# Performance work log

Hardware: AMD Instinct MI355X
Metric: run time of the kernel (lower is better)

The kernel has to match this reference:

```python
import jax, jax.numpy as jnp
import numpy as np
import math

DIM, DEPTH, HEADS, VOCAB, DMODEL = 200, 6, 10, 7, 512
DH = DIM // HEADS                      # 20
NBF = int(DH * math.log(DH))           # 59 FAVOR+ random features
FF = 4 * DIM                           # 800


def setup_inputs() -> dict:
    key = jax.random.key(0)
    ks = iter(jax.random.split(key, 32))
    s = 0.02
    inp = {
        'x': jax.random.normal(next(ks), (4, 16, 2048), jnp.float32),
        'token_emb': jax.random.normal(next(ks), (VOCAB, DIM)) * s,
        'ln1_g': jnp.ones((DEPTH, DIM)), 'ln1_b': jnp.zeros((DEPTH, DIM)),
        'wq': jax.random.normal(next(ks), (DEPTH, DIM, DIM)) * s, 'bq': jnp.zeros((DEPTH, DIM)),
        'wk': jax.random.normal(next(ks), (DEPTH, DIM, DIM)) * s, 'bk': jnp.zeros((DEPTH, DIM)),
        'wv': jax.random.normal(next(ks), (DEPTH, DIM, DIM)) * s, 'bv': jnp.zeros((DEPTH, DIM)),
        'proj': jax.random.normal(next(ks), (DEPTH, NBF, DH)),  # FAVOR+ projection (buffer)
        'wo': jax.random.normal(next(ks), (DEPTH, DIM, DIM)) * s, 'bo': jnp.zeros((DEPTH, DIM)),
        'ln2_g': jnp.ones((DEPTH, DIM)), 'ln2_b': jnp.zeros((DEPTH, DIM)),
        'ffw1': jax.random.normal(next(ks), (DEPTH, DIM, FF)) * s, 'ffb1': jnp.zeros((DEPTH, FF)),
        'ffw2': jax.random.normal(next(ks), (DEPTH, FF, DIM)) * s, 'ffb2': jnp.zeros((DEPTH, DIM)),
        'lnf_g': jnp.ones((DIM,)), 'lnf_b': jnp.zeros((DIM,)),
        'proj_w': jax.random.normal(next(ks), (DIM, DMODEL)) * s, 'proj_b': jnp.zeros((DMODEL,)),
    }
    return inp


def layer_norm(x, g, b, eps=1e-5):
    mu = x.mean(-1, keepdims=True)
    var = ((x - mu) ** 2).mean(-1, keepdims=True)
    return (x - mu) / jnp.sqrt(var + eps) * g + b


def softmax_kernel(data, proj, is_query, eps=1e-4):
    # data: (N,H,S,dh); proj: (m,dh)
    dn = data * (data.shape[-1] ** -0.25)
    dash = jnp.einsum('nhsd,md->nhsm', dn, proj)
    diag = 0.5 * jnp.sum(dn * dn, axis=-1, keepdims=True)
    mx = jnp.max(dash, axis=-1, keepdims=True) if is_query else jnp.max(dash)
    return (proj.shape[0] ** -0.5) * (jnp.exp(dash - diag - mx) + eps)


def attention(x, wq, bq, wk, bk, wv, bv, proj, wo, bo):
    N, S, D = x.shape
    split = lambda t: t.reshape(N, S, HEADS, DH).transpose(0, 2, 1, 3)
    q, k, v = split(x @ wq + bq), split(x @ wk + bk), split(x @ wv + bv)
    qp = softmax_kernel(q, proj, True)
    kp = softmax_kernel(k, proj, False)
    d_inv = 1.0 / jnp.einsum('nhsm,nhm->nhs', qp, kp.sum(axis=2))
    ctx = jnp.einsum('nhsm,nhsd->nhmd', kp, v)          # linear attention context
    out = jnp.einsum('nhsm,nhmd->nhsd', qp, ctx) * d_inv[..., None]
    return out.transpose(0, 2, 1, 3).reshape(N, S, D) @ wo + bo


def feedforward(x, w1, b1, w2, b2):
    return jax.nn.gelu(x @ w1 + b1, approximate=False) @ w2 + b2


def performer_forward(tokens, p):
    h = p['token_emb'][tokens]            # pos_emb is zeros (g2v_position_emb=False)
    x1, x2 = h, h                         # reversible net: x duplicated along channels
    for l in range(DEPTH):
        x1 = x1 + attention(layer_norm(x2, p['ln1_g'][l], p['ln1_b'][l]),
                            p['wq'][l], p['bq'][l], p['wk'][l], p['bk'][l],
                            p['wv'][l], p['bv'][l], p['proj'][l], p['wo'][l], p['bo'][l])
        x2 = x2 + feedforward(layer_norm(x1, p['ln2_g'][l], p['ln2_b'][l]),
                              p['ffw1'][l], p['ffb1'][l], p['ffw2'][l], p['ffb2'][l])
    h = 0.5 * (x1 + x2)                   # mean over the two reversible halves
    return layer_norm(h, p['lnf_g'], p['lnf_b'])


def reference(x, token_emb, ln1_g, ln1_b, wq, bq, wk, bk, wv, bv, proj, wo, bo,
              ln2_g, ln2_b, ffw1, ffb1, ffw2, ffb2, lnf_g, lnf_b, proj_w, proj_b):
    p = dict(token_emb=token_emb, ln1_g=ln1_g, ln1_b=ln1_b, wq=wq, bq=bq, wk=wk, bk=bk,
             wv=wv, bv=bv, proj=proj, wo=wo, bo=bo, ln2_g=ln2_g, ln2_b=ln2_b,
             ffw1=ffw1, ffb1=ffb1, ffw2=ffw2, ffb2=ffb2, lnf_g=lnf_g, lnf_b=lnf_b)
    B, Nt, T = x.shape
    xf = x.reshape(B * Nt, T)
    # torch.quantile on 1D positives -> bin_edges shape (1,4) != (T,4), so the
    # original falls back to zero bin edges; edges_plus = [0,0,0,0,inf], hence
    # token = 4 if value > 0 else 0, then + cls_token_id (1).
    tokens = jnp.where(xf > 0, 4, 0).astype(jnp.int32) + 1
    # chunk loop (chunk_size=512 samples) is identity math: run all at once
    enc = performer_forward(tokens, p)    # (B*Nt, T, DIM)
    pooled = enc.mean(axis=1)             # mean-pool over sequence
    out = pooled @ proj_w + proj_b
    return out.reshape(B, Nt, DMODEL)
```

## Files before the change

kernel.cpp:

```cpp
#include <hip/hip_runtime.h>
#include <hip/hip_bf16.h>
#include <math.h>

#define DEPTH   6
#define DIM     200
#define HEADS   10
#define DH      20
#define NBF     59
#define FFD     800
#define DMODEL  512
#define NSEQ    64
#define SEQ     2048
#define NTOK    (NSEQ*SEQ)
#define KPAD    224
#define BUFPAD  64
#define KNROW   40
#define VROW    136
#define KPROW   136
#define QPROW   72
#define CTXR    21
#define HSROW   132
#define PKV_E   (512*KPAD)
#define PQ_E    (256*KPAD)
#define PWO_E   (256*KPAD)
#define PF1_E   (896*KPAD)
#define PF2_E   (256*800)

typedef __hip_bfloat16 bf16;
typedef unsigned short u16;
typedef short s8v __attribute__((ext_vector_type(8)));
typedef short s4v __attribute__((ext_vector_type(4)));
typedef float f4v __attribute__((ext_vector_type(4)));

constexpr float SCALE = 0.4728708045015879f;
constexpr float RATIO = 0.1301889109808239f;
constexpr float KEPS  = 1e-4f;

__device__ __forceinline__ float b2f(bf16 v) { return __bfloat162float(v); }
__device__ __forceinline__ bf16 f2b(float v) { return __float2bfloat16(v); }
__device__ __forceinline__ float bfu(u16 u) {
    return __uint_as_float(((unsigned)u) << 16);
}
__device__ __forceinline__ u16 f2u(float v) {
    bf16 hb = __float2bfloat16(v);
    return *(u16*)&hb;
}
__device__ __forceinline__ float gelu_f(float x) {
    float inner = 0.7978845608028654f * (x + 0.044715f * x * x * x);
    float e = __expf(2.f * inner);
    return x * (1.f - 1.f / (e + 1.f));
}
__device__ __forceinline__ void gld_lds16(const short* g, short* l) {
    __builtin_amdgcn_global_load_lds(
        (const __attribute__((address_space(1))) void*)g,
        (__attribute__((address_space(3))) void*)l, 16, 0, 0);
}
#define MFMA16(a, b, c) __builtin_amdgcn_mfma_f32_16x16x32_bf16(a, b, c, 0, 0, 0)

__global__ void sentinel_kernel(float* out, float wsmb) {
    if (threadIdx.x == 0) out[0] = wsmb;
}

__global__ void zeropad_kernel(bf16* p1, bf16* p2, bf16* p3, bf16* p4) {
    int i = threadIdx.x;
    if (i < BUFPAD) {
        bf16 z = f2b(0.f);
        p1[i] = z; p2[i] = z; p3[i] = z; p4[i] = z;
    }
}

__global__ __launch_bounds__(256) void prep_layer(
        const float* __restrict__ wq, const float* __restrict__ wk,
        const float* __restrict__ wv, const float* __restrict__ wo,
        const float* __restrict__ f1, const float* __restrict__ f2,
        const float* __restrict__ g1, const float* __restrict__ b1,
        const float* __restrict__ g2, const float* __restrict__ b2,
        const float* __restrict__ bq, const float* __restrict__ bk,
        const float* __restrict__ bv, const float* __restrict__ f1b,
        bf16* __restrict__ pKV, bf16* __restrict__ pQ, bf16* __restrict__ pWO,
        bf16* __restrict__ pF1, bf16* __restrict__ pF2,
        float* __restrict__ uw) {
    int b = blockIdx.x, t = threadIdx.x;
    if (b < 448) {
        int idx = b * 256 + t;
        int row = idx / KPAD, k = idx % KPAD;
        float v = 0.f;
        if (k < DIM) {
            if (row < DIM) v = wk[(size_t)k * DIM + row] * g1[k];
            else if (row >= 256 && row < 256 + DIM)
                v = wv[(size_t)k * DIM + (row - 256)] * g1[k];
        }
        pKV[idx] = f2b(v);
    } else if (b < 672) {
        int idx = (b - 448) * 256 + t;
        int row = idx / KPAD, k = idx % KPAD;
        float v = (row < DIM && k < DIM) ? wq[(size_t)k * DIM + row] * g1[k] : 0.f;
        pQ[idx] = f2b(v);
    } else if (b < 896) {
        int idx = (b - 672) * 256 + t;
        int row = idx / KPAD, k = idx % KPAD;
        float v = (row < DIM && k < DIM) ? wo[(size_t)k * DIM + row] : 0.f;
        pWO[idx] = f2b(v);
    } else if (b < 1680) {
        int idx = (b - 896) * 256 + t;
        int row = idx / KPAD, k = idx % KPAD;
        float v = (row < FFD && k < DIM) ? f1[(size_t)k * FFD + row] * g2[k] : 0.f;
        pF1[idx] = f2b(v);
    } else if (b < 2480) {
        int idx = (b - 1680) * 256 + t;
        int row = idx / 800, k = idx % 800;
        float v = (row < DIM) ? f2[(size_t)k * DIM + row] : 0.f;
        pF2[idx] = f2b(v);
    } else if (b < 2482) {
        int j = b - 2480;
        const float* W    = j ? wv : wk;
        const float* bias = j ? bv : bk;
        int n = t;
        float su = 0.f, sw = 0.f;
        if (n < DIM) {
            for (int k = 0; k < DIM; ++k) {
                float wvv = W[(size_t)k * DIM + n];
                su += g1[k] * wvv;
                sw += b1[k] * wvv;
            }
            sw += bias[n];
        }
        uw[j * 256 + n] = su;
        uw[512 + j * 256 + n] = sw;
    } else if (b == 2482) {
        int n = t;
        float su = 0.f, sw = 0.f;
        if (n < DIM) {
            for (int k = 0; k < DIM; ++k) {
                float wvv = wq[(size_t)k * DIM + n];
                su += g1[k] * wvv;
                sw += b1[k] * wvv;
            }
            sw += bq[n];
        }
        uw[1024 + n] = su;
        uw[1280 + n] = sw;
    } else {
        int n = (b - 2483) * 256 + t;
        if (n < 896) {
            float su = 0.f, sw = 0.f;
            if (n < FFD) {
                for (int k = 0; k < DIM; ++k) {
                    float wvv = f1[(size_t)k * FFD + n];
                    su += g2[k] * wvv;
                    sw += b2[k] * wvv;
                }
                sw += f1b[n];
            }
            uw[1536 + n] = su;
            uw[2432 + n] = sw;
        }
    }
}

__global__ __launch_bounds__(256) void embed_kernel(const float* __restrict__ x,
        const float* __restrict__ emb, bf16* __restrict__ x1, bf16* __restrict__ x2) {
    int idx = blockIdx.x * 256 + threadIdx.x;
    if (idx >= NTOK * 25) return;
    int t = idx / 25, c = idx % 25;
    int row = (x[t] > 0.f) ? 5 : 1;
    const float4* e4 = (const float4*)(emb + row * DIM + c * 8);
    float4 e0 = e4[0], e1 = e4[1];
    s8v o;
    o[0] = (short)f2u(e0.x); o[1] = (short)f2u(e0.y);
    o[2] = (short)f2u(e0.z); o[3] = (short)f2u(e0.w);
    o[4] = (short)f2u(e1.x); o[5] = (short)f2u(e1.y);
    o[6] = (short)f2u(e1.z); o[7] = (short)f2u(e1.w);
    size_t off = (size_t)t * DIM + c * 8;
    *(s8v*)((short*)x1 + off) = o;
    *(s8v*)((short*)x2 + off) = o;
}

__global__ __launch_bounds__(256) void lnstats_kernel(const bf16* __restrict__ in,
        float* __restrict__ mu_o, float* __restrict__ rstd_o) {
    int lane = threadIdx.x & 63;
    size_t t = (size_t)blockIdx.x * 4 + (threadIdx.x >> 6);
    const u16* row = (const u16*)in + t * DIM;
    float v0 = 0.f, v1 = 0.f, v2 = 0.f, v3 = 0.f;
    if (lane < 50) {
        ushort4 u4 = ((const ushort4*)row)[lane];
        v0 = bfu(u4.x); v1 = bfu(u4.y); v2 = bfu(u4.z); v3 = bfu(u4.w);
    }
    float s = v0 + v1 + v2 + v3, qq = v0*v0 + v1*v1 + v2*v2 + v3*v3;
    #pragma unroll
    for (int o = 32; o > 0; o >>= 1) { s += __shfl_xor(s, o); qq += __shfl_xor(qq, o); }
    if (lane == 0) {
        float mu = s * (1.f / DIM);
        mu_o[t] = mu;
        rstd_o[t] = rsqrtf(qq * (1.f / DIM) - mu * mu + 1e-5f);
    }
}

__global__ __launch_bounds__(256) void finalln_kernel(const bf16* __restrict__ in1,
        const bf16* __restrict__ in2, const float* __restrict__ g,
        const float* __restrict__ b, bf16* __restrict__ out) {
    int lane = threadIdx.x & 63;
    size_t t = (size_t)blockIdx.x * 4 + (threadIdx.x >> 6);
    const u16* r1 = (const u16*)in1 + t * DIM;
    const u16* r2 = (const u16*)in2 + t * DIM;
    float v0 = 0.f, v1 = 0.f, v2 = 0.f, v3 = 0.f;
    if (lane < 50) {
        ushort4 a4 = ((const ushort4*)r1)[lane];
        ushort4 b4 = ((const ushort4*)r2)[lane];
        v0 = 0.5f * (bfu(a4.x) + bfu(b4.x));
        v1 = 0.5f * (bfu(a4.y) + bfu(b4.y));
        v2 = 0.5f * (bfu(a4.z) + bfu(b4.z));
        v3 = 0.5f * (bfu(a4.w) + bfu(b4.w));
    }
    float s = v0 + v1 + v2 + v3, qq = v0*v0 + v1*v1 + v2*v2 + v3*v3;
    #pragma unroll
    for (int o = 32; o > 0; o >>= 1) { s += __shfl_xor(s, o); qq += __shfl_xor(qq, o); }
    float mu = s * (1.f / DIM);
    float rstd = rsqrtf(qq * (1.f / DIM) - mu * mu + 1e-5f);
    if (lane < 50) {
        float4 g4 = ((const float4*)g)[lane];
        float4 b4f = ((const float4*)b)[lane];
        ushort4 o4;
        o4.x = f2u((v0 - mu) * rstd * g4.x + b4f.x);
        o4.y = f2u((v1 - mu) * rstd * g4.y + b4f.y);
        o4.z = f2u((v2 - mu) * rstd * g4.z + b4f.z);
        o4.w = f2u((v3 - mu) * rstd * g4.w + b4f.w);
        ((ushort4*)((u16*)out + t * DIM))[lane] = o4;
    }
}

template<int EPI, int LNE, int KV>
__global__ __launch_bounds__(256) void gemm_m(
        const bf16* __restrict__ A, const bf16* __restrict__ Bt,
        const float* __restrict__ wv_, const float* __restrict__ uv_,
        const float* __restrict__ mu, const float* __restrict__ rstd,
        bf16* __restrict__ C, bf16* __restrict__ C2,
        int M, int N, int K, int Kpad) {
    __shared__ __align__(16) short As[128 * 32];
    __shared__ __align__(16) short Bs[128 * 32];
    int bm = blockIdx.x * 128, bn = blockIdx.y * 128;
    int t = threadIdx.x, l = t & 63, w = t >> 6;
    int wr = (w >> 1) * 64, wc = (w & 1) * 64;
    int lr = l & 15, lk16 = l >> 4;
    f4v acc[4][4];
    #pragma unroll
    for (int i = 0; i < 4; ++i)
        #pragma unroll
        for (int j = 0; j < 4; ++j) acc[i][j] = (f4v){0.f, 0.f, 0.f, 0.f};

    const short* Ash = (const short*)A;
    const short* Bsh = (const short*)Bt;
    int srow0 = 32 * w + (l >> 2);
    int c16 = l & 3;
    for (int k0 = 0; k0 < Kpad; k0 += 32) {
        __syncthreads();
        #pragma unroll
        for (int j = 0; j < 2; ++j) {
            int row = srow0 + 16 * j;
            int xc = (c16 ^ ((row >> 1) & 3)) * 8;
            gld_lds16(Ash + (size_t)(bm + row) * K + k0 + xc,
                      &As[(32 * w + 16 * j) * 32]);
            gld_lds16(Bsh + (size_t)(bn + row) * Kpad + k0 + xc,
                      &Bs[(32 * w + 16 * j) * 32]);
        }
        __syncthreads();
        s8v a[4], b[4];
        #pragma unroll
        for (int fi = 0; fi < 4; ++fi) {
            int R = wr + fi * 16 + lr;
            a[fi] = *(const s8v*)&As[R * 32 + ((lk16 ^ ((R >> 1) & 3)) * 8)];
        }
        #pragma unroll
        for (int fj = 0; fj < 4; ++fj) {
            int R = wc + fj * 16 + lr;
            b[fj] = *(const s8v*)&Bs[R * 32 + ((lk16 ^ ((R >> 1) & 3)) * 8)];
        }
        #pragma unroll
        for (int fi = 0; fi < 4; ++fi)
            #pragma unroll
            for (int fj = 0; fj < 4; ++fj)
                acc[fi][fj] = MFMA16(a[fi], b[fj], acc[fi][fj]);
    }
    int r0 = (l >> 4) * 4;
    #pragma unroll
    for (int fi = 0; fi < 4; ++fi) {
        int rowb = bm + wr + fi * 16 + r0;
        float sr[4] = {1.f, 1.f, 1.f, 1.f}, tr[4] = {0.f, 0.f, 0.f, 0.f};
        if (LNE) {
            #pragma unroll
            for (int r = 0; r < 4; ++r) {
                sr[r] = rstd[rowb + r];
                tr[r] = mu[rowb + r] * sr[r];
            }
        }
        #pragma unroll
        for (int fj = 0; fj < 4; ++fj) {
            int col = bn + wc + fj * 16 + lr;
            if (KV) {
                int cc = col & 255;
                if (cc < DIM) {
                    bf16* dst = (col < 256) ? C : C2;
                    float ww = wv_[col], uu = uv_[col];
                    #pragma unroll
                    for (int r = 0; r < 4; ++r) {
                        size_t idx = (size_t)(rowb + r) * DIM + cc;
                        float v = sr[r] * acc[fi][fj][r] - tr[r] * uu + ww;
                        dst[idx] = f2b(v);
                    }
                }
            } else if (col < N) {
                float ww = wv_[col];
                float uu = LNE ? uv_[col] : 0.f;
                #pragma unroll
                for (int r = 0; r < 4; ++r) {
                    size_t idx = (size_t)(rowb + r) * N + col;
                    float v = LNE ? (sr[r] * acc[fi][fj][r] - tr[r] * uu + ww)
                                  : (acc[fi][fj][r] + ww);
                    if (EPI == 1) v += b2f(C[idx]);
                    if (EPI == 2) v = gelu_f(v);
                    C[idx] = f2b(v);
                }
            }
        }
    }
}

__global__ __launch_bounds__(256, 2) void ff_fused(
        const bf16* __restrict__ x1, const bf16* __restrict__ pF1,
        const bf16* __restrict__ pF2, const float* __restrict__ u1,
        const float* __restrict__ w1f, const float* __restrict__ fb2,
        const float* __restrict__ mu_in, const float* __restrict__ rstd_in,
        float* __restrict__ mu_out, float* __restrict__ rstd_out,
        bf16* __restrict__ x2) {
    __shared__ __align__(16) short Ax[64 * 256];
    __shared__ __align__(16) short Bs[2 * 128 * 32];
    __shared__ __align__(16) short hS[64 * HSROW];
    int bm = blockIdx.x * 64;
    int t = threadIdx.x, l = t & 63, w = t >> 6;
    int wrA = (w >> 1) * 32;
    int wcA = (w & 1) * 64;
    int wcB = (w & 1) * 128;
    int lr = l & 15, lk16 = l >> 4;
    int r0 = (l >> 4) * 4;
    const short* X1 = (const short*)x1;
    const short* F1 = (const short*)pF1;
    const short* F2 = (const short*)pF2;

    {
        int c = l & 31, rsub = l >> 5;
        #pragma unroll
        for (int j = 0; j < 8; ++j) {
            int row0 = w * 16 + j * 2;
            int row = row0 + rsub;
            gld_lds16(X1 + (size_t)(bm + row) * DIM + ((c ^ (row & 7)) * 8),
                      &Ax[row0 * 256]);
        }
    }

    f4v acc2[2][8];
    #pragma unroll
    for (int i = 0; i < 2; ++i)
        #pragma unroll
        for (int j = 0; j < 8; ++j) acc2[i][j] = (f4v){0.f, 0.f, 0.f, 0.f};

    int srow0 = 32 * w + (l >> 2);
    int c16 = l & 3;
    #pragma unroll 1
    for (int hc = 0; hc < 7; ++hc) {
        __syncthreads();
        #pragma unroll
        for (int j = 0; j < 2; ++j) {
            int row = srow0 + 16 * j;
            int xc = (c16 ^ ((row >> 1) & 3)) * 8;
            gld_lds16(F1 + (size_t)(hc * 128 + row) * KPAD + 0 + xc,
                      &Bs[(32 * w + 16 * j) * 32]);
        }
        __syncthreads();
        f4v acc1[2][4];
        #pragma unroll
        for (int i = 0; i < 2; ++i)
            #pragma unroll
            for (int j = 0; j < 4; ++j) acc1[i][j] = (f4v){0.f, 0.f, 0.f, 0.f};
        #pragma unroll 1
        for (int kt = 0; kt < 7; ++kt) {
            if (kt < 6) {
                int k0n = (kt + 1) * 32;
                int hb = ((kt + 1) & 1) * 4096;
                #pragma unroll
                for (int j = 0; j < 2; ++j) {
                    int row = srow0 + 16 * j;
                    int xc = (c16 ^ ((row >> 1) & 3)) * 8;
                    gld_lds16(F1 + (size_t)(hc * 128 + row) * KPAD + k0n + xc,
                              &Bs[hb + (32 * w + 16 * j) * 32]);
                }
            }
            int hb = (kt & 1) * 4096;
            s8v a[2], b[4];
            int cg = kt * 4 + lk16;
            #pragma unroll
            for (int fi = 0; fi < 2; ++fi) {
                int R = wrA + fi * 16 + lr;
                a[fi] = *(const s8v*)&Ax[R * 256 + ((cg ^ (R & 7)) * 8)];
            }
            #pragma unroll
            for (int fj = 0; fj < 4; ++fj) {
                int R = wcA + fj * 16 + lr;
                b[fj] = *(const s8v*)&Bs[hb + R * 32 + ((lk16 ^ ((R >> 1) & 3)) * 8)];
            }
            #pragma unroll
            for (int fi = 0; fi < 2; ++fi)
                #pragma unroll
                for (int fj = 0; fj < 4; ++fj)
                    acc1[fi][fj] = MFMA16(a[fi], b[fj], acc1[fi][fj]);
            __syncthreads();
        }
        #pragma unroll
        for (int fi = 0; fi < 2; ++fi) {
            int rowL = wrA + fi * 16 + r0;
            f4v rs = *(const f4v*)&rstd_in[bm + rowL];
            f4v mm = *(const f4v*)&mu_in[bm + rowL];
            #pragma unroll
            for (int fj = 0; fj < 4; ++fj) {
                int col = wcA + fj * 16 + lr;
                int gcol = hc * 128 + col;
                float uu = u1[gcol], ww = w1f[gcol];
                #pragma unroll
                for (int r = 0; r < 4; ++r) {
                    float v = rs[r] * acc1[fi][fj][r] - mm[r] * rs[r] * uu + ww;
                    v = gelu_f(v);
                    int rr = rowL + r;
                    hS[rr * HSROW + (((col >> 3) ^ (rr & 7)) * 8) + (col & 7)]
                        = (short)f2u(v);
                }
            }
        }
        #pragma unroll 1
        for (int ks = 0; ks < 4; ++ks) {
            __syncthreads();
            #pragma unroll
            for (int j = 0; j < 4; ++j) {
                int row = (w * 4 + j) * 16 + (l >> 2);
                int xc = (c16 ^ ((row >> 1) & 3)) * 8;
                gld_lds16(F2 + (size_t)row * 800 + hc * 128 + ks * 32 + xc,
                          &Bs[(w * 4 + j) * 16 * 32]);
            }
            __syncthreads();
            s8v a[2];
            int cg = ks * 4 + lk16;
            #pragma unroll
            for (int fi = 0; fi < 2; ++fi) {
                int R = wrA + fi * 16 + lr;
                a[fi] = *(const s8v*)&hS[R * HSROW + ((cg ^ (R & 7)) * 8)];
            }
            #pragma unroll
            for (int fj = 0; fj < 8; ++fj) {
                int Br = wcB + fj * 16 + lr;
                s8v bfr = *(const s8v*)&Bs[Br * 32 + ((lk16 ^ ((Br >> 1) & 3)) * 8)];
                #pragma unroll
                for (int fi = 0; fi < 2; ++fi)
                    acc2[fi][fj] = MFMA16(a[fi], bfr, acc2[fi][fj]);
            }
        }
    }
    __syncthreads();
    float* sp = (float*)hS;
    float rsum[2][4], rsq[2][4];
    #pragma unroll
    for (int fi = 0; fi < 2; ++fi)
        #pragma unroll
        for (int r = 0; r < 4; ++r) { rsum[fi][r] = 0.f; rsq[fi][r] = 0.f; }
    #pragma unroll
    for (int fi = 0; fi < 2; ++fi) {
        int rowb = bm + wrA + fi * 16 + r0;
        #pragma unroll
        for (int fj = 0; fj < 8; ++fj) {
            int col = wcB + fj * 16 + lr;
            if (col < DIM) {
                float bb = fb2[col];
                #pragma unroll
                for (int r = 0; r < 4; ++r) {
                    size_t idx = (size_t)(rowb + r) * DIM + col;
                    float v = acc2[fi][fj][r] + bb + b2f(x2[idx]);
                    x2[idx] = f2b(v);
                    rsum[fi][r] += v;
                    rsq[fi][r] += v * v;
                }
            }
        }
    }
    #pragma unroll
    for (int fi = 0; fi < 2; ++fi)
        #pragma unroll
        for (int r = 0; r < 4; ++r) {
            float s = rsum[fi][r], q = rsq[fi][r];
            #pragma unroll
            for (int o = 8; o > 0; o >>= 1) {
                s += __shfl_xor(s, o);
                q += __shfl_xor(q, o);
            }
            rsum[fi][r] = s; rsq[fi][r] = q;
        }
    if (lr == 0) {
        #pragma unroll
        for (int fi = 0; fi < 2; ++fi)
            #pragma unroll
            for (int r = 0; r < 4; ++r) {
                int rowL = wrA + fi * 16 + r0 + r;
                sp[rowL * 4 + (w & 1) * 2 + 0] = rsum[fi][r];
                sp[rowL * 4 + (w & 1) * 2 + 1] = rsq[fi][r];
            }
    }
    __syncthreads();
    if (t < 64) {
        float s = sp[t * 4 + 0] + sp[t * 4 + 2];
        float q = sp[t * 4 + 1] + sp[t * 4 + 3];
        float mu = s * (1.f / DIM);
        mu_out[bm + t] = mu;
        rstd_out[bm + t] = rsqrtf(q * (1.f / DIM) - mu * mu + 1e-5f);
    }
}

__global__ __launch_bounds__(256) void kvctx_mfma(const bf16* __restrict__ k,
        const bf16* __restrict__ v, const float* __restrict__ proj,
        float* __restrict__ ctxg) {
    __shared__ __align__(16) short ph[64 * KNROW];
    __shared__ __align__(16) short pl[64 * KNROW];
    __shared__ __align__(16) short knh[128 * KNROW];
    __shared__ __align__(16) short knl[128 * KNROW];
    __shared__ __align__(16) short vT[32 * VROW];
    __shared__ __align__(16) short kp[64 * KPROW];
    __shared__ __align__(16) float diag[128];
    __shared__ float wmax[4];
    int nh = blockIdx.x, n = nh / HEADS, h = nh % HEADS;
    int t = threadIdx.x, l = t & 63, w = t >> 6;
    int lr = l & 15, lk = (l >> 4) * 8, l4 = (l >> 4) * 4;
    for (int i = t; i < 64 * 32; i += 256) {
        int m = i >> 5, d = i & 31;
        float val = (m < NBF && d < DH) ? proj[m * DH + d] : 0.f;
        u16 hi = f2u(val);
        ph[m * KNROW + d] = (short)hi;
        pl[m * KNROW + d] = (short)f2u(val - bfu(hi));
    }
    for (int i = t; i < 128 * 12; i += 256) {
        int s = i / 12, d = 20 + i % 12;
        knh[s * KNROW + d] = 0; knl[s * KNROW + d] = 0;
    }
    for (int i = t; i < 12 * 128; i += 256) {
        int d = 20 + (i >> 7), s = i & 127;
        vT[d * VROW + s] = (short)((d == 20) ? f2u(1.0f) : 0);
    }
    s8v ones;
    #pragma unroll
    for (int i = 0; i < 8; ++i) ones[i] = (short)f2u(1.0f);
    float Mrun = -3.0e38f;
    f4v cd0 = {0.f,0.f,0.f,0.f}, cd1 = {0.f,0.f,0.f,0.f};
    f4v vs0 = {0.f,0.f,0.f,0.f}, vs1 = {0.f,0.f,0.f,0.f};
    for (int c = 0; c < 16; ++c) {
        int s0 = c * 128;
        __syncthreads();
        if (t < 128) {
            int s = t;
            const u16* kr = (const u16*)k + ((size_t)(n * SEQ + s0 + s)) * DIM + h * DH;
            float dg = 0.f;
            #pragma unroll
            for (int q5 = 0; q5 < 5; ++q5) {
                ushort4 u4 = ((const ushort4*)kr)[q5];
                float f0 = bfu(u4.x) * SCALE, f1 = bfu(u4.y) * SCALE;
                float f2_ = bfu(u4.z) * SCALE, f3 = bfu(u4.w) * SCALE;
                dg += f0*f0 + f1*f1 + f2_*f2_ + f3*f3;
                u16 h0 = f2u(f0), h1 = f2u(f1), h2 = f2u(f2_), h3 = f2u(f3);
                s4v hv = {(short)h0, (short)h1, (short)h2, (short)h3};
                *(s4v*)&knh[s * KNROW + q5 * 4] = hv;
                s4v lv = {(short)f2u(f0 - bfu(h0)), (short)f2u(f1 - bfu(h1)),
                          (short)f2u(f2_ - bfu(h2)), (short)f2u(f3 - bfu(h3))};
                *(s4v*)&knl[s * KNROW + q5 * 4] = lv;
            }
            diag[s] = 0.5f * dg;
        } else {
            int s = t - 128;
            const u16* vr = (const u16*)v + ((size_t)(n * SEQ + s0 + s)) * DIM + h * DH;
            #pragma unroll
            for (int q5 = 0; q5 < 5; ++q5) {
                ushort4 u4 = ((const ushort4*)vr)[q5];
                vT[(q5 * 4 + 0) * VROW + s] = (short)u4.x;
                vT[(q5 * 4 + 1) * VROW + s] = (short)u4.y;
                vT[(q5 * 4 + 2) * VROW + s] = (short)u4.z;
                vT[(q5 * 4 + 3) * VROW + s] = (short)u4.w;
            }
        }
        __syncthreads();
        s8v ah0 = *(const s8v*)&knh[(32 * w + lr) * KNROW + lk];
        s8v al0 = *(const s8v*)&knl[(32 * w + lr) * KNROW + lk];
        s8v ah1 = *(const s8v*)&knh[(32 * w + 16 + lr) * KNROW + lk];
        s8v al1 = *(const s8v*)&knl[(32 * w + 16 + lr) * KNROW + lk];
        f4v dg0 = *(const f4v*)&diag[32 * w + l4];
        f4v dg1 = *(const f4v*)&diag[32 * w + 16 + l4];
        f4v D0[4], D1[4];
        #pragma unroll
        for (int mt = 0; mt < 4; ++mt) {
            s8v bh = *(const s8v*)&ph[(mt * 16 + lr) * KNROW + lk];
            s8v bl = *(const s8v*)&pl[(mt * 16 + lr) * KNROW + lk];
            f4v d0 = {0.f, 0.f, 0.f, 0.f}, d1 = {0.f, 0.f, 0.f, 0.f};
            d0 = MFMA16(ah0, bh, d0); d0 = MFMA16(ah0, bl, d0); d0 = MFMA16(al0, bh, d0);
            d1 = MFMA16(ah1, bh, d1); d1 = MFMA16(ah1, bl, d1); d1 = MFMA16(al1, bh, d1);
            D0[mt] = d0; D1[mt] = d1;
        }
        float mm = -3.0e38f;
        #pragma unroll
        for (int mt = 0; mt < 4; ++mt) {
            int lim = (mt < 3) ? 16 : (NBF - 48);
            if (lr < lim) {
                #pragma unroll
                for (int r = 0; r < 4; ++r)
                    mm = fmaxf(mm, fmaxf(D0[mt][r], D1[mt][r]));
            }
        }
        #pragma unroll
        for (int o = 32; o > 0; o >>= 1) mm = fmaxf(mm, __shfl_xor(mm, o));
        if (l == 0) wmax[w] = mm;
        __syncthreads();
        float Mnew = fmaxf(fmaxf(wmax[0], wmax[1]), fmaxf(wmax[2], wmax[3]));
        Mnew = fmaxf(Mrun, Mnew);
        float scl = __expf(Mrun - Mnew);
        #pragma unroll
        for (int r = 0; r < 4; ++r) { cd0[r] *= scl; cd1[r] *= scl; }
        Mrun = Mnew;
        #pragma unroll
        for (int mt = 0; mt < 4; ++mt) {
            int m = mt * 16 + lr;
            bool valid = m < NBF;
            s4v o0, o1;
            #pragma unroll
            for (int r = 0; r < 4; ++r) {
                float kp0 = valid ? __expf(D0[mt][r] - dg0[r] - Mnew) : 0.f;
                float kp1 = valid ? __expf(D1[mt][r] - dg1[r] - Mnew) : 0.f;
                o0[r] = (short)f2u(kp0);
                o1[r] = (short)f2u(kp1);
            }
            *(s4v*)&kp[m * KPROW + 32 * w + l4] = o0;
            *(s4v*)&kp[m * KPROW + 32 * w + 16 + l4] = o1;
        }
        __syncthreads();
        #pragma unroll
        for (int ks = 0; ks < 4; ++ks) {
            s8v a  = *(const s8v*)&kp[(16 * w + lr) * KPROW + ks * 32 + lk];
            s8v b0 = *(const s8v*)&vT[lr * VROW + ks * 32 + lk];
            s8v b1 = *(const s8v*)&vT[(16 + lr) * VROW + ks * 32 + lk];
            cd0 = MFMA16(a, b0, cd0);
            cd1 = MFMA16(a, b1, cd1);
            vs0 = MFMA16(ones, b0, vs0);
            vs1 = MFMA16(ones, b1, vs1);
        }
    }
    float* cg = ctxg + (size_t)nh * CTXR * 64;
    int m0 = 16 * w + l4;
    f4v r0v, r1v;
    #pragma unroll
    for (int r = 0; r < 4; ++r) {
        r0v[r] = RATIO * (cd0[r] + KEPS * vs0[r]);
        r1v[r] = RATIO * (cd1[r] + KEPS * vs1[r]);
    }
    *(f4v*)&cg[lr * 64 + m0] = r0v;
    if (lr < 5) *(f4v*)&cg[(16 + lr) * 64 + m0] = r1v;
}

__global__ __launch_bounds__(256) void qattn_mfma(const bf16* __restrict__ q,
        const float* __restrict__ proj, const float* __restrict__ ctxg,
        bf16* __restrict__ ao) {
    __shared__ __align__(16) short ph[64 * KNROW];
    __shared__ __align__(16) short pl[64 * KNROW];
    __shared__ __align__(16) short qnh[128 * KNROW];
    __shared__ __align__(16) short qnl[128 * KNROW];
    __shared__ __align__(16) short qp[128 * QPROW];
    __shared__ __align__(16) short cT[32 * QPROW];
    __shared__ __align__(16) float dgs[128];
    __shared__ __align__(16) float osf[128][22];
    int b = blockIdx.x;
    int nh = b >> 1, sc = b & 1;
    int n = nh / HEADS, h = nh % HEADS;
    int t = threadIdx.x, l = t & 63, w = t >> 6;
    int lr = l & 15, lk = (l >> 4) * 8, l4 = (l >> 4) * 4;
    for (int i = t; i < 64 * 32; i += 256) {
        int m = i >> 5, d = i & 31;
        float val = (m < NBF && d < DH) ? proj[m * DH + d] : 0.f;
        u16 hi = f2u(val);
        ph[m * KNROW + d] = (short)hi;
        pl[m * KNROW + d] = (short)f2u(val - bfu(hi));
    }
    for (int i = t; i < 128 * 12; i += 256) {
        int s = i / 12, d = 20 + i % 12;
        qnh[s * KNROW + d] = 0; qnl[s * KNROW + d] = 0;
    }
    for (int i = t; i < 32 * 64; i += 256) {
        int d = i >> 6, m = i & 63;
        float val = (d < CTXR) ? ctxg[(size_t)nh * CTXR * 64 + d * 64 + m] : 0.f;
        cT[d * QPROW + m] = (short)f2u(val);
    }
    for (int c = 0; c < 8; ++c) {
        int s0 = (sc * 8 + c) * 128;
        __syncthreads();
        if (t < 128) {
            int s = t;
            const u16* qr = (const u16*)q + ((size_t)(n * SEQ + s0 + s)) * DIM + h * DH;
            float dg = 0.f;
            #pragma unroll
            for (int q5 = 0; q5 < 5; ++q5) {
                ushort4 u4 = ((const ushort4*)qr)[q5];
                float f0 = bfu(u4.x) * SCALE, f1 = bfu(u4.y) * SCALE;
                float f2_ = bfu(u4.z) * SCALE, f3 = bfu(u4.w) * SCALE;
                dg += f0*f0 + f1*f1 + f2_*f2_ + f3*f3;
                u16 h0 = f2u(f0), h1 = f2u(f1), h2 = f2u(f2_), h3 = f2u(f3);
                s4v hv = {(short)h0, (short)h1, (short)h2, (short)h3};
                *(s4v*)&qnh[s * KNROW + q5 * 4] = hv;
                s4v lv = {(short)f2u(f0 - bfu(h0)), (short)f2u(f1 - bfu(h1)),
                          (short)f2u(f2_ - bfu(h2)), (short)f2u(f3 - bfu(h3))};
                *(s4v*)&qnl[s * KNROW + q5 * 4] = lv;
            }
            dgs[s] = 0.5f * dg;
        }
        __syncthreads();
        s8v ah0 = *(const s8v*)&qnh[(32 * w + lr) * KNROW + lk];
        s8v al0 = *(const s8v*)&qnl[(32 * w + lr) * KNROW + lk];
        s8v ah1 = *(const s8v*)&qnh[(32 * w + 16 + lr) * KNROW + lk];
        s8v al1 = *(const s8v*)&qnl[(32 * w + 16 + lr) * KNROW + lk];
        f4v D0[4], D1[4];
        #pragma unroll
        for (int mt = 0; mt < 4; ++mt) {
            s8v bh = *(const s8v*)&ph[(mt * 16 + lr) * KNROW + lk];
            s8v bl = *(const s8v*)&pl[(mt * 16 + lr) * KNROW + lk];
            f4v d0 = {0.f, 0.f, 0.f, 0.f}, d1 = {0.f, 0.f, 0.f, 0.f};
            d0 = MFMA16(ah0, bh, d0); d0 = MFMA16(ah0, bl, d0); d0 = MFMA16(al0, bh, d0);
            d1 = MFMA16(ah1, bh, d1); d1 = MFMA16(ah1, bl, d1); d1 = MFMA16(al1, bh, d1);
            D0[mt] = d0; D1[mt] = d1;
        }
        f4v dg0 = *(const f4v*)&dgs[32 * w + l4];
        f4v dg1 = *(const f4v*)&dgs[32 * w + 16 + l4];
        float mx0[4], mx1[4];
        #pragma unroll
        for (int r = 0; r < 4; ++r) {
            float v3 = (lr < NBF - 48) ? D0[3][r] : -3.4e38f;
            float mm = fmaxf(fmaxf(D0[0][r], D0[1][r]), fmaxf(D0[2][r], v3));
            mm = fmaxf(mm, __shfl_xor(mm, 1));
            mm = fmaxf(mm, __shfl_xor(mm, 2));
            mm = fmaxf(mm, __shfl_xor(mm, 4));
            mm = fmaxf(mm, __shfl_xor(mm, 8));
            mx0[r] = mm;
            float u3 = (lr < NBF - 48) ? D1[3][r] : -3.4e38f;
            float nn = fmaxf(fmaxf(D1[0][r], D1[1][r]), fmaxf(D1[2][r], u3));
            nn = fmaxf(nn, __shfl_xor(nn, 1));
            nn = fmaxf(nn, __shfl_xor(nn, 2));
            nn = fmaxf(nn, __shfl_xor(nn, 4));
            nn = fmaxf(nn, __shfl_xor(nn, 8));
            mx1[r] = nn;
        }
        #pragma unroll
        for (int mt = 0; mt < 4; ++mt) {
            int m = mt * 16 + lr;
            bool valid = m < NBF;
            #pragma unroll
            for (int r = 0; r < 4; ++r) {
                float p0 = valid ? RATIO * (__expf(D0[mt][r] - dg0[r] - mx0[r]) + KEPS) : 0.f;
                float p1 = valid ? RATIO * (__expf(D1[mt][r] - dg1[r] - mx1[r]) + KEPS) : 0.f;
                qp[(32 * w + l4 + r) * QPROW + m] = (short)f2u(p0);
                qp[(32 * w + 16 + l4 + r) * QPROW + m] = (short)f2u(p1);
            }
        }
        __syncthreads();
        f4v o00 = {0.f,0.f,0.f,0.f}, o01 = {0.f,0.f,0.f,0.f};
        f4v o10 = {0.f,0.f,0.f,0.f}, o11 = {0.f,0.f,0.f,0.f};
        #pragma unroll
        for (int ks = 0; ks < 2; ++ks) {
            s8v a0 = *(const s8v*)&qp[(32 * w + lr) * QPROW + ks * 32 + lk];
            s8v a1 = *(const s8v*)&qp[(32 * w + 16 + lr) * QPROW + ks * 32 + lk];
            s8v b0 = *(const s8v*)&cT[lr * QPROW + ks * 32 + lk];
            s8v b1 = *(const s8v*)&cT[(16 + lr) * QPROW + ks * 32 + lk];
            o00 = MFMA16(a0, b0, o00); o01 = MFMA16(a0, b1, o01);
            o10 = MFMA16(a1, b0, o10); o11 = MFMA16(a1, b1, o11);
        }
        #pragma unroll
        for (int r = 0; r < 4; ++r) {
            osf[32 * w + l4 + r][lr] = o00[r];
            osf[32 * w + 16 + l4 + r][lr] = o10[r];
            if (lr < 5) {
                osf[32 * w + l4 + r][16 + lr] = o01[r];
                osf[32 * w + 16 + l4 + r][16 + lr] = o11[r];
            }
        }
        __syncthreads();
        if (t < 128) osf[t][21] = 1.f / osf[t][20];
        __syncthreads();
        int tokb = n * SEQ + s0;
        for (int idx = t; idx < 128 * 10; idx += 256) {
            int row = idx / 10, seg = idx % 10;
            float di = osf[row][21];
            ushort2 o2;
            o2.x = f2u(osf[row][seg * 2] * di);
            o2.y = f2u(osf[row][seg * 2 + 1] * di);
            *(ushort2*)((u16*)ao + (size_t)(tokb + row) * DIM + h * DH + seg * 2) = o2;
        }
    }
}

__global__ __launch_bounds__(256) void pool1_kernel(const bf16* __restrict__ hn,
        float* __restrict__ partial) {
    int n = blockIdx.x / 16, c = blockIdx.x % 16;
    int d = threadIdx.x;
    if (d >= DIM) return;
    float acc = 0.f;
    const bf16* base = hn + ((size_t)n * SEQ + c * 128) * DIM + d;
    for (int s = 0; s < 128; ++s) acc += b2f(base[(size_t)s * DIM]);
    partial[(size_t)blockIdx.x * DIM + d] = acc;
}

__global__ __launch_bounds__(256) void pool2_kernel(const float* __restrict__ partial,
        float* __restrict__ pooled) {
    int n = blockIdx.x, d = threadIdx.x;
    if (d >= DIM) return;
    float acc = 0.f;
    for (int c = 0; c < 16; ++c) acc += partial[(size_t)(n * 16 + c) * DIM + d];
    pooled[n * DIM + d] = acc * (1.f / SEQ);
}

__global__ __launch_bounds__(512) void finalproj_kernel(const float* __restrict__ pooled,
        const float* __restrict__ pw, const float* __restrict__ pb,
        float* __restrict__ out) {
    __shared__ float ps[DIM];
    int n = blockIdx.x;
    for (int i = threadIdx.x; i < DIM; i += 512) ps[i] = pooled[n * DIM + i];
    __syncthreads();
    int j = threadIdx.x;
    float acc = pb[j];
    for (int d = 0; d < DIM; ++d) acc += ps[d] * pw[d * DMODEL + j];
    out[n * DMODEL + j] = acc;
}

extern "C" void kernel_launch(void* const* d_in, const int* in_sizes, int n_in,
                              void* d_out, int out_size, void* d_ws, size_t ws_size,
                              hipStream_t stream) {
    (void)in_sizes; (void)n_in; (void)out_size;
    const float* x    = (const float*)d_in[0];
    const float* emb  = (const float*)d_in[1];
    const float* ln1g = (const float*)d_in[2];
    const float* ln1b = (const float*)d_in[3];
    const float* wq   = (const float*)d_in[4];
    const float* bq   = (const float*)d_in[5];
    const float* wk   = (const float*)d_in[6];
    const float* bk   = (const float*)d_in[7];
    const float* wv   = (const float*)d_in[8];
    const float* bv   = (const float*)d_in[9];
    const float* proj = (const float*)d_in[10];
    const float* wo   = (const float*)d_in[11];
    const float* bo   = (const float*)d_in[12];
    const float* ln2g = (const float*)d_in[13];
    const float* ln2b = (const float*)d_in[14];
    const float* ffw1 = (const float*)d_in[15];
    const float* ffb1 = (const float*)d_in[16];
    const float* ffw2 = (const float*)d_in[17];
    const float* ffb2 = (const float*)d_in[18];
    const float* lnfg = (const float*)d_in[19];
    const float* lnfb = (const float*)d_in[20];
    const float* pw   = (const float*)d_in[21];
    const float* pb   = (const float*)d_in[22];
    float* out = (float*)d_out;

    const size_t A_ = (size_t)NTOK * DIM;
    bf16* x1 = (bf16*)d_ws;
    bf16* x2 = x1 + A_ + BUFPAD;
    bf16* b3 = x2 + A_ + BUFPAD;
    bf16* b4 = b3 + A_ + BUFPAD;
    bf16* pKV = b4 + A_ + BUFPAD;
    bf16* pQ  = pKV + PKV_E;
    bf16* pWO = pQ + PQ_E;
    bf16* pF1 = pWO + PWO_E;
    bf16* pF2 = pF1 + PF1_E;
    float* muB   = (float*)(pF2 + PF2_E);
    float* rstdB = muB + NTOK;
    float* muC   = rstdB + NTOK;
    float* rstdC = muC + NTOK;
    float* uw    = rstdC + NTOK;
    float* ctxg  = uw + 3328;
    float* wsend = ctxg + (size_t)NSEQ * HEADS * CTXR * 64;

    float* ukv = uw,        *wkv = uw + 512;
    float* uq  = uw + 1024, *wqf = uw + 1280;
    float* u1  = uw + 1536, *w1f = uw + 2432;

    size_t need = (char*)wsend - (char*)d_ws;
    if (ws_size < need) {
        sentinel_kernel<<<1, 64, 0, stream>>>(out, (float)(ws_size >> 20));
        return;
    }

    zeropad_kernel<<<1, 64, 0, stream>>>(x1 + A_, x2 + A_, b3 + A_, b4 + A_);
    embed_kernel<<<(NTOK * 25 + 255) / 256, 256, 0, stream>>>(x, emb, x1, x2);
    lnstats_kernel<<<NTOK / 4, 256, 0, stream>>>(x2, muB, rstdB);

    dim3 gkv(NTOK / 128, 4);
    dim3 gd(NTOK / 128, 2);
    for (int l = 0; l < DEPTH; ++l) {
        const float* wq_l = wq + (size_t)l * DIM * DIM;
        const float* wk_l = wk + (size_t)l * DIM * DIM;
        const float* wv_l = wv + (size_t)l * DIM * DIM;
        const float* wo_l = wo + (size_t)l * DIM * DIM;
        const float* f1_l = ffw1 + (size_t)l * DIM * FFD;
        const float* f2_l = ffw2 + (size_t)l * FFD * DIM;
        const float* pj_l = proj + (size_t)l * NBF * DH;
        const float* g1 = ln1g + l * DIM, *b1 = ln1b + l * DIM;
        const float* g2 = ln2g + l * DIM, *b2 = ln2b + l * DIM;

        prep_layer<<<2487, 256, 0, stream>>>(wq_l, wk_l, wv_l, wo_l, f1_l, f2_l,
                g1, b1, g2, b2, bq + l * DIM, bk + l * DIM, bv + l * DIM,
                ffb1 + l * FFD, pKV, pQ, pWO, pF1, pF2, uw);

        gemm_m<0, 1, 1><<<gkv, 256, 0, stream>>>(x2, pKV, wkv, ukv, muB, rstdB,
                b3, b4, NTOK, 512, DIM, KPAD);
        kvctx_mfma<<<NSEQ * HEADS, 256, 0, stream>>>(b3, b4, pj_l, ctxg);
        gemm_m<0, 1, 0><<<gd, 256, 0, stream>>>(x2, pQ, wqf, uq, muB, rstdB,
                b3, nullptr, NTOK, DIM, DIM, KPAD);
        qattn_mfma<<<NSEQ * HEADS * 2, 256, 0, stream>>>(b3, pj_l, ctxg, b4);
        gemm_m<1, 0, 0><<<gd, 256, 0, stream>>>(b4, pWO, bo + l * DIM, nullptr,
                nullptr, nullptr, x1, nullptr, NTOK, DIM, DIM, KPAD);

        lnstats_kernel<<<NTOK / 4, 256, 0, stream>>>(x1, muC, rstdC);
        ff_fused<<<NTOK / 64, 256, 0, stream>>>(x1, pF1, pF2, u1, w1f,
                ffb2 + l * DIM, muC, rstdC, muB, rstdB, x2);
    }

    finalln_kernel<<<NTOK / 4, 256, 0, stream>>>(x1, x2, lnfg, lnfb, b3);
    float* partial = muB;
    float* pooled  = muB + (size_t)NSEQ * 16 * DIM;
    pool1_kernel<<<NSEQ * 16, 256, 0, stream>>>(b3, partial);
    pool2_kernel<<<NSEQ, 256, 0, stream>>>(partial, pooled);
    finalproj_kernel<<<NSEQ, 512, 0, stream>>>(pooled, pw, pb, out);
}
```

Baseline: 4.330 ms.

## Hoist FF input tile into registers and alias LDS to raise occupancy

The 64x224 input tile of the fused feed-forward kernel is read once from LDS into registers (areg[7][2]) before the main loop. The LDS region that held it is then reused for the weight staging buffer and GELU hidden tile through a union. This cuts LDS per block so three blocks can fit per CU, and launch bounds change from 2 to 3 to match. The cost is 56 extra VGPRs of held fragments under a tighter register budget, which risks spills, and the sync points move to keep the aliased buffers safe.

```diff
diff --git a/kernel.cpp b/kernel.cpp
--- a/kernel.cpp
+++ b/kernel.cpp
@@ -325,16 +325,20 @@
     }
 }
 
-__global__ __launch_bounds__(256, 2) void ff_fused(
+struct SmemFF {
+    union {
+        short Ax[64 * 256];
+        struct { short Bs[2 * 128 * 32]; short hS[64 * HSROW]; } p;
+    };
+};
+__global__ __launch_bounds__(256, 3) void ff_fused(
         const bf16* __restrict__ x1, const bf16* __restrict__ pF1,
         const bf16* __restrict__ pF2, const float* __restrict__ u1,
         const float* __restrict__ w1f, const float* __restrict__ fb2,
         const float* __restrict__ mu_in, const float* __restrict__ rstd_in,
         float* __restrict__ mu_out, float* __restrict__ rstd_out,
         bf16* __restrict__ x2) {
-    __shared__ __align__(16) short Ax[64 * 256];
-    __shared__ __align__(16) short Bs[2 * 128 * 32];
-    __shared__ __align__(16) short hS[64 * HSROW];
+    __shared__ __align__(16) SmemFF sm;
     int bm = blockIdx.x * 64;
     int t = threadIdx.x, l = t & 63, w = t >> 6;
     int wrA = (w >> 1) * 32;
@@ -353,9 +357,21 @@
             int row0 = w * 16 + j * 2;
             int row = row0 + rsub;
             gld_lds16(X1 + (size_t)(bm + row) * DIM + ((c ^ (row & 7)) * 8),
-                      &Ax[row0 * 256]);
-        }
-    }
+                      &sm.Ax[row0 * 256]);
+        }
+    }
+    __syncthreads();
+    s8v areg[7][2];
+    #pragma unroll
+    for (int kt = 0; kt < 7; ++kt) {
+        int cg = kt * 4 + lk16;
+        #pragma unroll
+        for (int fi = 0; fi < 2; ++fi) {
+            int R = wrA + fi * 16 + lr;
+            areg[kt][fi] = *(const s8v*)&sm.Ax[R * 256 + ((cg ^ (R & 7)) * 8)];
+        }
+    }
+    __syncthreads();
 
     f4v acc2[2][8];
     #pragma unroll
@@ -367,13 +383,12 @@
     int c16 = l & 3;
     #pragma unroll 1
     for (int hc = 0; hc < 7; ++hc) {
-        __syncthreads();
         #pragma unroll
         for (int j = 0; j < 2; ++j) {
             int row = srow0 + 16 * j;
             int xc = (c16 ^ ((row >> 1) & 3)) * 8;
             gld_lds16(F1 + (size_t)(hc * 128 + row) * KPAD + 0 + xc,
-                      &Bs[(32 * w + 16 * j) * 32]);
+                      &sm.p.Bs[(32 * w + 16 * j) * 32]);
         }
         __syncthreads();
         f4v acc1[2][4];
@@ -391,27 +406,21 @@
                     int row = srow0 + 16 * j;
                     int xc = (c16 ^ ((row >> 1) & 3)) * 8;
                     gld_lds16(F1 + (size_t)(hc * 128 + row) * KPAD + k0n + xc,
-                              &Bs[hb + (32 * w + 16 * j) * 32]);
+                              &sm.p.Bs[hb + (32 * w + 16 * j) * 32]);
                 }
             }
             int hb = (kt & 1) * 4096;
-            s8v a[2], b[4];
-            int cg = kt * 4 + lk16;
-            #pragma unroll
-            for (int fi = 0; fi < 2; ++fi) {
-                int R = wrA + fi * 16 + lr;
-                a[fi] = *(const s8v*)&Ax[R * 256 + ((cg ^ (R & 7)) * 8)];
-            }
+            s8v b[4];
             #pragma unroll
             for (int fj = 0; fj < 4; ++fj) {
                 int R = wcA + fj * 16 + lr;
-                b[fj] = *(const s8v*)&Bs[hb + R * 32 + ((lk16 ^ ((R >> 1) & 3)) * 8)];
+                b[fj] = *(const s8v*)&sm.p.Bs[hb + R * 32 + ((lk16 ^ ((R >> 1) & 3)) * 8)];
             }
             #pragma unroll
             for (int fi = 0; fi < 2; ++fi)
                 #pragma unroll
                 for (int fj = 0; fj < 4; ++fj)
-                    acc1[fi][fj] = MFMA16(a[fi], b[fj], acc1[fi][fj]);
+                    acc1[fi][fj] = MFMA16(areg[kt][fi], b[fj], acc1[fi][fj]);
             __syncthreads();
         }
         #pragma unroll
@@ -429,7 +438,7 @@
                     float v = rs[r] * acc1[fi][fj][r] - mm[r] * rs[r] * uu + ww;
                     v = gelu_f(v);
                     int rr = rowL + r;
-                    hS[rr * HSROW + (((col >> 3) ^ (rr & 7)) * 8) + (col & 7)]
+                    sm.p.hS[rr * HSROW + (((col >> 3) ^ (rr & 7)) * 8) + (col & 7)]
                         = (short)f2u(v);
                 }
             }
@@ -442,7 +451,7 @@
                 int row = (w * 4 + j) * 16 + (l >> 2);
                 int xc = (c16 ^ ((row >> 1) & 3)) * 8;
                 gld_lds16(F2 + (size_t)row * 800 + hc * 128 + ks * 32 + xc,
-                          &Bs[(w * 4 + j) * 16 * 32]);
+                          &sm.p.Bs[(w * 4 + j) * 16 * 32]);
             }
             __syncthreads();
             s8v a[2];
@@ -450,20 +459,20 @@
             #pragma unroll
             for (int fi = 0; fi < 2; ++fi) {
                 int R = wrA + fi * 16 + lr;
-                a[fi] = *(const s8v*)&hS[R * HSROW + ((cg ^ (R & 7)) * 8)];
+                a[fi] = *(const s8v*)&sm.p.hS[R * HSROW + ((cg ^ (R & 7)) * 8)];
             }
             #pragma unroll
             for (int fj = 0; fj < 8; ++fj) {
                 int Br = wcB + fj * 16 + lr;
-                s8v bfr = *(const s8v*)&Bs[Br * 32 + ((lk16 ^ ((Br >> 1) & 3)) * 8)];
+                s8v bfr = *(const s8v*)&sm.p.Bs[Br * 32 + ((lk16 ^ ((Br >> 1) & 3)) * 8)];
                 #pragma unroll
                 for (int fi = 0; fi < 2; ++fi)
                     acc2[fi][fj] = MFMA16(a[fi], bfr, acc2[fi][fj]);
             }
         }
-    }
-    __syncthreads();
-    float* sp = (float*)hS;
+        __syncthreads();
+    }
+    float* sp = (float*)sm.p.hS;
     float rsum[2][4], rsq[2][4];
     #pragma unroll
     for (int fi = 0; fi < 2; ++fi)
```

After: 5.691 ms. +31.4%, slower.
